# Performance work log

Measured on AMD Instinct MI355X. Metric: run time of the kernel, lower is better.

## Reference

```python
import jax, jax.numpy as jnp
import numpy as np

B, N, D = 64, 1024, 1024

def setup_inputs() -> dict:
    key = jax.random.key(0)
    k1, k2, k3, k4, k5 = jax.random.split(key, 5)
    s = 1.0 / np.sqrt(D)
    return {
        "h_t": jax.random.normal(k1, (B, D), dtype=jnp.float32),
        "keys": jax.random.normal(k2, (B, N, D), dtype=jnp.float32),
        "W_h": jax.random.uniform(k3, (D, D), jnp.float32, -s, s),
        "W_k": jax.random.uniform(k4, (D, D), jnp.float32, -s, s),
        "v": jax.random.uniform(k5, (D,), jnp.float32, -s, s),
    }

def reference(h_t, keys, W_h, W_k, v):
    # W_h(h_t): [B, D]; W_k(keys): [B, N, D]  (nn.Linear computes x @ W.T)
    qh = h_t @ W_h.T                       # [B, D]
    kh = jnp.einsum('bnd,ed->bne', keys, W_k)  # [B, N, D]
    energy = jnp.tanh(qh[:, None, :] + kh)     # [B, N, D]
    scores = jnp.einsum('bnd,d->bn', energy, v)  # [B, N]
    alpha = jax.nn.softmax(scores, axis=-1)      # [B, N]
    context = jnp.einsum('bn,bnd->bd', alpha, keys)  # [B, D]
    return (context, alpha)
```

## Files before the change

### kernel.cpp

```cpp
#include <hip/hip_runtime.h>
#include <math.h>

#define BB 64
#define NN 1024
#define DD 1024

typedef __bf16 bf16x8 __attribute__((ext_vector_type(8)));
typedef _Float16 f16x8 __attribute__((ext_vector_type(8)));
typedef _Float16 f16x4 __attribute__((ext_vector_type(4)));
typedef float f32x4 __attribute__((ext_vector_type(4)));
typedef unsigned short u16x8 __attribute__((ext_vector_type(8)));

#define GLOAD_LDS16(g, l)                                                  \
    __builtin_amdgcn_global_load_lds(                                      \
        (const __attribute__((address_space(1))) unsigned int*)(g),        \
        (__attribute__((address_space(3))) unsigned int*)(l), 16, 0, 0)

__device__ __forceinline__ float fast_tanh(float x) {
    return 1.f - 2.f / (__expf(2.f * x) + 1.f);
}


__global__ __launch_bounds__(256) void cvt_keys(const float* __restrict__ keys,
                                                _Float16* __restrict__ keysT) {
    const int b = blockIdx.y;
    const int nt = blockIdx.x;
    const int t = threadIdx.x;
    const float4* src = (const float4*)(keys + ((size_t)b * NN + nt * 128) * DD);
    _Float16* dst = keysT + (((size_t)b * 8 + nt) * 32) * 4096;
    const int kt = t >> 3;
    const int kc = (t & 7) * 4;
    _Float16* dcol = dst + (size_t)kt * 4096 + kc;
#pragma unroll 4
    for (int n = 0; n < 128; ++n) {
        float4 v4 = src[n * 256 + t];
        f16x4 h = {(_Float16)v4.x, (_Float16)v4.y, (_Float16)v4.z, (_Float16)v4.w};
        *(f16x4*)(dcol + n * 32) = h;
    }
}

__global__ __launch_bounds__(256) void cvt_wk(const float* __restrict__ W_k,
                                              _Float16* __restrict__ wkT) {
    const int et = blockIdx.x;
    const int t = threadIdx.x;
    const float4* src = (const float4*)(W_k + (size_t)et * 128 * DD);
    _Float16* dst = wkT + ((size_t)et * 32) * 4096;
    const int kt = t >> 3;
    const int kc = (t & 7) * 4;
    _Float16* dcol = dst + (size_t)kt * 4096 + kc;
#pragma unroll 4
    for (int n = 0; n < 128; ++n) {
        float4 v4 = src[n * 256 + t];
        f16x4 h = {(_Float16)v4.x, (_Float16)v4.y, (_Float16)v4.z, (_Float16)v4.w};
        *(f16x4*)(dcol + n * 32) = h;
    }
}

__global__ __launch_bounds__(256) void qh_fast(const float* __restrict__ h_t,
                                               const float* __restrict__ W_h,
                                               float* __restrict__ qh,
                                               float* __restrict__ scores) {
    __shared__ float hs[4 * 1024];
    const int ec = blockIdx.x;
    const int bg = blockIdx.y;
    const int t = threadIdx.x;
    const int flat = bg * 4 + ec;
#pragma unroll
    for (int j = 0; j < 4; ++j) scores[flat * 1024 + j * 256 + t] = 0.f;
    const float4* hsrc = (const float4*)(h_t + (size_t)bg * 4 * DD);
    float4* hdst = (float4*)hs;
    for (int i = t; i < 1024; i += 256) hdst[i] = hsrc[i];
    __syncthreads();
    const int e = ec * 256 + t;
    const float4* wrow = (const float4*)(W_h + (size_t)e * DD);
    float a0 = 0.f, a1 = 0.f, a2 = 0.f, a3 = 0.f;
#pragma unroll 2
    for (int k4 = 0; k4 < 256; ++k4) {
        float4 wv = wrow[k4];
        const float* h0 = &hs[4 * k4];
        a0 = fmaf(wv.x, h0[0], a0); a0 = fmaf(wv.y, h0[1], a0);
        a0 = fmaf(wv.z, h0[2], a0); a0 = fmaf(wv.w, h0[3], a0);
        const float* h1 = &hs[1024 + 4 * k4];
        a1 = fmaf(wv.x, h1[0], a1); a1 = fmaf(wv.y, h1[1], a1);
        a1 = fmaf(wv.z, h1[2], a1); a1 = fmaf(wv.w, h1[3], a1);
        const float* h2 = &hs[2048 + 4 * k4];
        a2 = fmaf(wv.x, h2[0], a2); a2 = fmaf(wv.y, h2[1], a2);
        a2 = fmaf(wv.z, h2[2], a2); a2 = fmaf(wv.w, h2[3], a2);
        const float* h3 = &hs[3072 + 4 * k4];
        a3 = fmaf(wv.x, h3[0], a3); a3 = fmaf(wv.y, h3[1], a3);
        a3 = fmaf(wv.z, h3[2], a3); a3 = fmaf(wv.w, h3[3], a3);
    }
    const int b0 = bg * 4;
    qh[(b0 + 0) * DD + e] = a0;
    qh[(b0 + 1) * DD + e] = a1;
    qh[(b0 + 2) * DD + e] = a2;
    qh[(b0 + 3) * DD + e] = a3;
}

__global__ __launch_bounds__(256) void scores_mfma(const _Float16* __restrict__ keysT,
                                                   const _Float16* __restrict__ wkT,
                                                   const float* __restrict__ v,
                                                   const float* __restrict__ qh,
                                                   float* __restrict__ scores) {
    __shared__ _Float16 As[128 * 32];
    __shared__ _Float16 Bs[128 * 32];
    __shared__ float vs[128];
    __shared__ float qs[128];
    __shared__ float red[128][2];

    const int tid = threadIdx.x;
    const int cp = blockIdx.x;
    const int rt = blockIdx.y;
    const int b = rt >> 3;
    const int nt = rt & 7;
    const int e0 = cp * 128;

    if (tid < 128) {
        vs[tid] = v[e0 + tid];
        qs[tid] = qh[b * DD + e0 + tid];
    }

    const char* Abase = (const char*)(keysT + (((size_t)b * 8 + nt) * 32) * 4096);
    const char* Bbase = (const char*)(wkT + ((size_t)cp * 32) * 4096);

    const int w = tid >> 6;
    const int lane = tid & 63;
    const int wm = w & 1;
    const int we = w >> 1;
    const int lcol = lane & 15;
    const int quad = lane >> 4;
    const int soff = w * 2048 + lane * 16;

    f32x4 acc[4][4];
#pragma unroll
    for (int mi = 0; mi < 4; ++mi)
#pragma unroll
        for (int ni = 0; ni < 4; ++ni) acc[mi][ni] = (f32x4){0.f, 0.f, 0.f, 0.f};

    for (int kt = 0; kt < 32; ++kt) {
        __syncthreads();
        const char* ag = Abase + (size_t)kt * 8192 + soff;
        const char* bg = Bbase + (size_t)kt * 8192 + soff;
        char* al_ = (char*)As + soff;
        char* bl_ = (char*)Bs + soff;
        GLOAD_LDS16(ag, al_);
        GLOAD_LDS16(ag + 1024, al_ + 1024);
        GLOAD_LDS16(bg, bl_);
        GLOAD_LDS16(bg + 1024, bl_ + 1024);
        __syncthreads();

        f16x8 af[4], bf[4];
#pragma unroll
        for (int mi = 0; mi < 4; ++mi)
            af[mi] = *(const f16x8*)&As[(wm * 64 + mi * 16 + lcol) * 32 + quad * 8];
#pragma unroll
        for (int ni = 0; ni < 4; ++ni)
            bf[ni] = *(const f16x8*)&Bs[(we * 64 + ni * 16 + lcol) * 32 + quad * 8];
#pragma unroll
        for (int mi = 0; mi < 4; ++mi)
#pragma unroll
            for (int ni = 0; ni < 4; ++ni)
                acc[mi][ni] = __builtin_amdgcn_mfma_f32_16x16x32_f16(af[mi], bf[ni], acc[mi][ni], 0, 0, 0);
    }

    float part[4][4];
#pragma unroll
    for (int mi = 0; mi < 4; ++mi)
#pragma unroll
        for (int r = 0; r < 4; ++r) part[mi][r] = 0.f;
#pragma unroll
    for (int mi = 0; mi < 4; ++mi)
#pragma unroll
        for (int ni = 0; ni < 4; ++ni) {
            const int e = we * 64 + ni * 16 + lcol;
            const float vv = vs[e];
            const float qv = qs[e];
#pragma unroll
            for (int r = 0; r < 4; ++r)
                part[mi][r] += vv * fast_tanh(qv + acc[mi][ni][r]);
        }
#pragma unroll
    for (int mi = 0; mi < 4; ++mi)
#pragma unroll
        for (int r = 0; r < 4; ++r) {
            float p = part[mi][r];
            p += __shfl_xor(p, 1);
            p += __shfl_xor(p, 2);
            p += __shfl_xor(p, 4);
            p += __shfl_xor(p, 8);
            if (lcol == 0) red[wm * 64 + mi * 16 + quad * 4 + r][we] = p;
        }
    __syncthreads();
    if (tid < 128) atomicAdd(&scores[b * NN + nt * 128 + tid], red[tid][0] + red[tid][1]);
}

__global__ __launch_bounds__(256) void softmax_kernel(const float* __restrict__ scores,
                                                      float* __restrict__ alpha,
                                                      float* __restrict__ context) {
    const int b = blockIdx.x;
    const int t = threadIdx.x;
#pragma unroll
    for (int j = 0; j < 4; ++j) context[b * DD + t + 256 * j] = 0.f;
    float x[4];
    float m = -1e30f;
#pragma unroll
    for (int j = 0; j < 4; ++j) {
        x[j] = scores[b * NN + t + 256 * j];
        m = fmaxf(m, x[j]);
    }
#pragma unroll
    for (int mask = 32; mask >= 1; mask >>= 1) m = fmaxf(m, __shfl_xor(m, mask));
    __shared__ float wred[4];
    __shared__ float wsum[4];
    const int wv = t >> 6;
    if ((t & 63) == 0) wred[wv] = m;
    __syncthreads();
    m = fmaxf(fmaxf(wred[0], wred[1]), fmaxf(wred[2], wred[3]));
    float s = 0.f;
#pragma unroll
    for (int j = 0; j < 4; ++j) {
        x[j] = expf(x[j] - m);
        s += x[j];
    }
#pragma unroll
    for (int mask = 32; mask >= 1; mask >>= 1) s += __shfl_xor(s, mask);
    if ((t & 63) == 0) wsum[wv] = s;
    __syncthreads();
    s = wsum[0] + wsum[1] + wsum[2] + wsum[3];
    const float inv = 1.f / s;
#pragma unroll
    for (int j = 0; j < 4; ++j) alpha[b * NN + t + 256 * j] = x[j] * inv;
}

__global__ __launch_bounds__(256) void context_f16(const _Float16* __restrict__ keysT,
                                                   const float* __restrict__ alpha,
                                                   float* __restrict__ context) {
    const int b = blockIdx.y;
    const int nc = blockIdx.x;
    const int t = threadIdx.x;
    __shared__ float al[128];
    if (t < 128) al[t] = alpha[b * NN + nc * 128 + t];
    __syncthreads();
    const _Float16* chunk = keysT + (((size_t)b * 8 + nc) * 32) * 4096;
    const int kt = t >> 3;
    const int kc = (t & 7) * 4;
    const _Float16* p = chunk + (size_t)kt * 4096 + kc;
    float4 acc = {0.f, 0.f, 0.f, 0.f};
#pragma unroll 4
    for (int n = 0; n < 128; ++n) {
        const float a = al[n];
        f16x4 kv = *(const f16x4*)(p + n * 32);
        acc.x = fmaf(a, (float)kv[0], acc.x);
        acc.y = fmaf(a, (float)kv[1], acc.y);
        acc.z = fmaf(a, (float)kv[2], acc.z);
        acc.w = fmaf(a, (float)kv[3], acc.w);
    }
    float* cp = context + b * DD + kt * 32 + kc;
    atomicAdd(cp + 0, acc.x);
    atomicAdd(cp + 1, acc.y);
    atomicAdd(cp + 2, acc.z);
    atomicAdd(cp + 3, acc.w);
}

__global__ __launch_bounds__(256) void qh_fb(const float* __restrict__ h_t,
                                             const float* __restrict__ W_h,
                                             float* __restrict__ qh,
                                             float* __restrict__ scores) {
    __shared__ float hs[DD];
    const int b = blockIdx.y;
    const int e = blockIdx.x * 256 + threadIdx.x;
    scores[(blockIdx.y * 4 + blockIdx.x) * 256 + threadIdx.x] = 0.f;
    for (int i = threadIdx.x; i < DD; i += 256) hs[i] = h_t[b * DD + i];
    __syncthreads();
    const float4* wrow = (const float4*)(W_h + (size_t)e * DD);
    float acc = 0.f;
#pragma unroll 4
    for (int k4 = 0; k4 < DD / 4; ++k4) {
        float4 w = wrow[k4];
        acc = fmaf(w.x, hs[4 * k4 + 0], acc);
        acc = fmaf(w.y, hs[4 * k4 + 1], acc);
        acc = fmaf(w.z, hs[4 * k4 + 2], acc);
        acc = fmaf(w.w, hs[4 * k4 + 3], acc);
    }
    qh[b * DD + e] = acc;
}

#define SPAD 40
__device__ __forceinline__ void split16(const float4* __restrict__ src,
                                        unsigned short* hi, unsigned short* lo) {
    float x[16];
    float4 v0 = src[0], v1 = src[1], v2 = src[2], v3 = src[3];
    x[0] = v0.x; x[1] = v0.y; x[2] = v0.z; x[3] = v0.w;
    x[4] = v1.x; x[5] = v1.y; x[6] = v1.z; x[7] = v1.w;
    x[8] = v2.x; x[9] = v2.y; x[10] = v2.z; x[11] = v2.w;
    x[12] = v3.x; x[13] = v3.y; x[14] = v3.z; x[15] = v3.w;
#pragma unroll
    for (int i = 0; i < 16; ++i) {
        unsigned int u = __float_as_uint(x[i]);
        hi[i] = (unsigned short)(u >> 16);
        float hif = __uint_as_float(u & 0xFFFF0000u);
        float lof = x[i] - hif;
        lo[i] = (unsigned short)(__float_as_uint(lof) >> 16);
    }
}

__global__ __launch_bounds__(256, 2) void scores_fb(const float* __restrict__ keys,
                                                    const float* __restrict__ W_k,
                                                    const float* __restrict__ v,
                                                    const float* __restrict__ qh,
                                                    float* __restrict__ scores) {
    __shared__ unsigned short Ah[128 * SPAD];
    __shared__ unsigned short Al[128 * SPAD];
    __shared__ unsigned short Bh[128 * SPAD];
    __shared__ unsigned short Bl[128 * SPAD];
    __shared__ float vs[128];
    __shared__ float qs[128];
    __shared__ float red[128][2];

    const int tid = threadIdx.x;
    const int cp = blockIdx.x;
    const int rt = blockIdx.y;
    const int b = rt >> 3;
    const int n0 = (rt & 7) * 128;
    const int e0 = cp * 128;
    if (tid < 128) {
        vs[tid] = v[e0 + tid];
        qs[tid] = qh[b * DD + e0 + tid];
    }
    const float* Ag = keys + ((size_t)b * NN + n0) * DD;
    const float* Bg = W_k + (size_t)e0 * DD;
    const int w = tid >> 6;
    const int lane = tid & 63;
    const int wm = w & 1;
    const int we = w >> 1;
    const int lcol = lane & 15;
    const int quad = lane >> 4;
    f32x4 acc[4][4];
#pragma unroll
    for (int mi = 0; mi < 4; ++mi)
#pragma unroll
        for (int ni = 0; ni < 4; ++ni) acc[mi][ni] = (f32x4){0.f, 0.f, 0.f, 0.f};
    const int srow = tid >> 1;
    const int sseg = tid & 1;
    float4 pa[4], pb[4];
    {
        const float4* as = (const float4*)(Ag + (size_t)srow * DD + sseg * 16);
        const float4* bs = (const float4*)(Bg + (size_t)srow * DD + sseg * 16);
#pragma unroll
        for (int i = 0; i < 4; ++i) { pa[i] = as[i]; pb[i] = bs[i]; }
    }
    for (int kt = 0; kt < DD / 32; ++kt) {
        __syncthreads();
        {
            unsigned short hi[16], lo[16];
            split16(pa, hi, lo);
            u16x8* dh = (u16x8*)&Ah[srow * SPAD + sseg * 16];
            u16x8* dl = (u16x8*)&Al[srow * SPAD + sseg * 16];
            dh[0] = *(u16x8*)&hi[0]; dh[1] = *(u16x8*)&hi[8];
            dl[0] = *(u16x8*)&lo[0]; dl[1] = *(u16x8*)&lo[8];
            split16(pb, hi, lo);
            u16x8* eh = (u16x8*)&Bh[srow * SPAD + sseg * 16];
            u16x8* el = (u16x8*)&Bl[srow * SPAD + sseg * 16];
            eh[0] = *(u16x8*)&hi[0]; eh[1] = *(u16x8*)&hi[8];
            el[0] = *(u16x8*)&lo[0]; el[1] = *(u16x8*)&lo[8];
        }
        if (kt + 1 < DD / 32) {
            const int k0 = (kt + 1) * 32;
            const float4* as = (const float4*)(Ag + (size_t)srow * DD + k0 + sseg * 16);
            const float4* bs = (const float4*)(Bg + (size_t)srow * DD + k0 + sseg * 16);
#pragma unroll
            for (int i = 0; i < 4; ++i) { pa[i] = as[i]; pb[i] = bs[i]; }
        }
        __syncthreads();
        bf16x8 ah[4], al2[4], bh[4], bl2[4];
#pragma unroll
        for (int mi = 0; mi < 4; ++mi) {
            const int r = wm * 64 + mi * 16 + lcol;
            ah[mi] = *(const bf16x8*)&Ah[r * SPAD + quad * 8];
            al2[mi] = *(const bf16x8*)&Al[r * SPAD + quad * 8];
        }
#pragma unroll
        for (int ni = 0; ni < 4; ++ni) {
            const int r = we * 64 + ni * 16 + lcol;
            bh[ni] = *(const bf16x8*)&Bh[r * SPAD + quad * 8];
            bl2[ni] = *(const bf16x8*)&Bl[r * SPAD + quad * 8];
        }
#pragma unroll
        for (int mi = 0; mi < 4; ++mi)
#pragma unroll
            for (int ni = 0; ni < 4; ++ni) {
                acc[mi][ni] = __builtin_amdgcn_mfma_f32_16x16x32_bf16(ah[mi], bh[ni], acc[mi][ni], 0, 0, 0);
                acc[mi][ni] = __builtin_amdgcn_mfma_f32_16x16x32_bf16(ah[mi], bl2[ni], acc[mi][ni], 0, 0, 0);
                acc[mi][ni] = __builtin_amdgcn_mfma_f32_16x16x32_bf16(al2[mi], bh[ni], acc[mi][ni], 0, 0, 0);
            }
    }
    float part[4][4];
#pragma unroll
    for (int mi = 0; mi < 4; ++mi)
#pragma unroll
        for (int r = 0; r < 4; ++r) part[mi][r] = 0.f;
#pragma unroll
    for (int mi = 0; mi < 4; ++mi)
#pragma unroll
        for (int ni = 0; ni < 4; ++ni) {
            const int e = we * 64 + ni * 16 + lcol;
            const float vv = vs[e];
            const float qv = qs[e];
#pragma unroll
            for (int r = 0; r < 4; ++r)
                part[mi][r] += vv * fast_tanh(qv + acc[mi][ni][r]);
        }
#pragma unroll
    for (int mi = 0; mi < 4; ++mi)
#pragma unroll
        for (int r = 0; r < 4; ++r) {
            float p = part[mi][r];
            p += __shfl_xor(p, 1);
            p += __shfl_xor(p, 2);
            p += __shfl_xor(p, 4);
            p += __shfl_xor(p, 8);
            if (lcol == 0) red[wm * 64 + mi * 16 + quad * 4 + r][we] = p;
        }
    __syncthreads();
    if (tid < 128) atomicAdd(&scores[b * NN + n0 + tid], red[tid][0] + red[tid][1]);
}

__global__ __launch_bounds__(256) void context_fb(const float* __restrict__ keys,
                                                  const float* __restrict__ alpha,
                                                  float* __restrict__ context) {
    const int b = blockIdx.y;
    const int nc = blockIdx.x;
    const int t = threadIdx.x;
    __shared__ float al[128];
    if (t < 128) al[t] = alpha[b * NN + nc * 128 + t];
    __syncthreads();
    const float4* kp = (const float4*)(keys + ((size_t)b * NN + nc * 128) * DD);
    float4 acc = {0.f, 0.f, 0.f, 0.f};
#pragma unroll 4
    for (int n = 0; n < 128; ++n) {
        const float a = al[n];
        float4 kv = kp[(size_t)n * (DD / 4) + t];
        acc.x = fmaf(a, kv.x, acc.x);
        acc.y = fmaf(a, kv.y, acc.y);
        acc.z = fmaf(a, kv.z, acc.z);
        acc.w = fmaf(a, kv.w, acc.w);
    }
    float* cp = context + b * DD + 4 * t;
    atomicAdd(cp + 0, acc.x);
    atomicAdd(cp + 1, acc.y);
    atomicAdd(cp + 2, acc.z);
    atomicAdd(cp + 3, acc.w);
}

extern "C" void kernel_launch(void* const* d_in, const int* in_sizes, int n_in,
                              void* d_out, int out_size, void* d_ws, size_t ws_size,
                              hipStream_t stream) {
    const float* h_t = (const float*)d_in[0];
    const float* keys = (const float*)d_in[1];
    const float* W_h = (const float*)d_in[2];
    const float* W_k = (const float*)d_in[3];
    const float* v = (const float*)d_in[4];

    float* context = (float*)d_out;
    float* alpha = (float*)d_out + BB * DD;
    float* qh = (float*)d_ws;
    float* scores = (float*)d_ws + BB * DD;

    const size_t wkT_off = (size_t)2 * BB * DD * sizeof(float);
    const size_t keysT_off = wkT_off + (size_t)DD * DD * 2;
    const size_t need = keysT_off + (size_t)BB * NN * DD * 2;

    if (ws_size >= need) {
        _Float16* wkT = (_Float16*)((char*)d_ws + wkT_off);
        _Float16* keysT = (_Float16*)((char*)d_ws + keysT_off);
        cvt_keys<<<dim3(8, BB), 256, 0, stream>>>(keys, keysT);
        cvt_wk<<<dim3(8), 256, 0, stream>>>(W_k, wkT);
        qh_fast<<<dim3(4, 16), 256, 0, stream>>>(h_t, W_h, qh, scores);
        scores_mfma<<<dim3(8, 512), 256, 0, stream>>>(keysT, wkT, v, qh, scores);
        softmax_kernel<<<BB, 256, 0, stream>>>(scores, alpha, context);
        context_f16<<<dim3(8, BB), 256, 0, stream>>>(keysT, alpha, context);
    } else {
        qh_fb<<<dim3(4, BB), 256, 0, stream>>>(h_t, W_h, qh, scores);
        scores_fb<<<dim3(8, 512), 256, 0, stream>>>(keys, W_k, v, qh, scores);
        softmax_kernel<<<BB, 256, 0, stream>>>(scores, alpha, context);
        context_fb<<<dim3(8, BB), 256, 0, stream>>>(keys, alpha, context);
    }
}
```

Before: 677.1 us.

## Merge conversion kernels, double K-step in MFMA loop, rework qh and context

```diff
diff --git a/kernel.cpp b/kernel.cpp
--- a/kernel.cpp
+++ b/kernel.cpp
@@ -21,38 +21,29 @@
 }
 
 
-__global__ __launch_bounds__(256) void cvt_keys(const float* __restrict__ keys,
-                                                _Float16* __restrict__ keysT) {
-    const int b = blockIdx.y;
+__global__ __launch_bounds__(256) void cvt_all(const float* __restrict__ keys,
+                                               const float* __restrict__ W_k,
+                                               _Float16* __restrict__ keysT,
+                                               _Float16* __restrict__ wkT) {
     const int nt = blockIdx.x;
+    const int bb = blockIdx.y;
     const int t = threadIdx.x;
-    const float4* src = (const float4*)(keys + ((size_t)b * NN + nt * 128) * DD);
-    _Float16* dst = keysT + (((size_t)b * 8 + nt) * 32) * 4096;
-    const int kt = t >> 3;
-    const int kc = (t & 7) * 4;
-    _Float16* dcol = dst + (size_t)kt * 4096 + kc;
-#pragma unroll 4
-    for (int n = 0; n < 128; ++n) {
-        float4 v4 = src[n * 256 + t];
-        f16x4 h = {(_Float16)v4.x, (_Float16)v4.y, (_Float16)v4.z, (_Float16)v4.w};
-        *(f16x4*)(dcol + n * 32) = h;
-    }
-}
-
-__global__ __launch_bounds__(256) void cvt_wk(const float* __restrict__ W_k,
-                                              _Float16* __restrict__ wkT) {
-    const int et = blockIdx.x;
-    const int t = threadIdx.x;
-    const float4* src = (const float4*)(W_k + (size_t)et * 128 * DD);
-    _Float16* dst = wkT + ((size_t)et * 32) * 4096;
-    const int kt = t >> 3;
-    const int kc = (t & 7) * 4;
-    _Float16* dcol = dst + (size_t)kt * 4096 + kc;
-#pragma unroll 4
-    for (int n = 0; n < 128; ++n) {
-        float4 v4 = src[n * 256 + t];
-        f16x4 h = {(_Float16)v4.x, (_Float16)v4.y, (_Float16)v4.z, (_Float16)v4.w};
-        *(f16x4*)(dcol + n * 32) = h;
+    const float* src = (bb == 64) ? (W_k + (size_t)nt * 128 * DD)
+                                  : (keys + ((size_t)bb * NN + nt * 128) * DD);
+    _Float16* dst = (bb == 64) ? (wkT + (size_t)nt * 32 * 4096)
+                               : (keysT + (((size_t)bb * 8 + nt) * 32) * 4096);
+    for (int kt = 0; kt < 32; ++kt) {
+#pragma unroll
+        for (int r = 0; r < 2; ++r) {
+            const int p = r * 2048 + t * 8;
+            const int n = p >> 5;
+            const int k = p & 31;
+            const float4* s4 = (const float4*)(src + (size_t)n * DD + kt * 32 + k);
+            float4 a = s4[0], b4 = s4[1];
+            f16x8 h = {(_Float16)a.x,  (_Float16)a.y,  (_Float16)a.z,  (_Float16)a.w,
+                       (_Float16)b4.x, (_Float16)b4.y, (_Float16)b4.z, (_Float16)b4.w};
+            *(f16x8*)(dst + (size_t)kt * 4096 + p) = h;
+        }
     }
 }
 
@@ -60,59 +51,64 @@
                                                const float* __restrict__ W_h,
                                                float* __restrict__ qh,
                                                float* __restrict__ scores) {
-    __shared__ float hs[4 * 1024];
-    const int ec = blockIdx.x;
+    __shared__ float hs[8 * 1024];
+    __shared__ float red2[128][8];
+    const int et = blockIdx.x;
     const int bg = blockIdx.y;
     const int t = threadIdx.x;
-    const int flat = bg * 4 + ec;
-#pragma unroll
-    for (int j = 0; j < 4; ++j) scores[flat * 1024 + j * 256 + t] = 0.f;
-    const float4* hsrc = (const float4*)(h_t + (size_t)bg * 4 * DD);
+    const int bid = bg * 8 + et;
+#pragma unroll
+    for (int j = 0; j < 4; ++j) scores[bid * 1024 + j * 256 + t] = 0.f;
+    const int b0 = bg * 8;
+    const float4* hsrc = (const float4*)(h_t + (size_t)b0 * DD);
     float4* hdst = (float4*)hs;
-    for (int i = t; i < 1024; i += 256) hdst[i] = hsrc[i];
-    __syncthreads();
-    const int e = ec * 256 + t;
-    const float4* wrow = (const float4*)(W_h + (size_t)e * DD);
-    float a0 = 0.f, a1 = 0.f, a2 = 0.f, a3 = 0.f;
-#pragma unroll 2
-    for (int k4 = 0; k4 < 256; ++k4) {
+    for (int i = t; i < 2048; i += 256) hdst[i] = hsrc[i];
+    __syncthreads();
+    const int el = t & 127;
+    const int half = t >> 7;
+    const int e = et * 128 + el;
+    const float4* wrow = (const float4*)(W_h + (size_t)e * DD) + half * 128;
+    float p[8];
+#pragma unroll
+    for (int bi = 0; bi < 8; ++bi) p[bi] = 0.f;
+    for (int k4 = 0; k4 < 128; ++k4) {
         float4 wv = wrow[k4];
-        const float* h0 = &hs[4 * k4];
-        a0 = fmaf(wv.x, h0[0], a0); a0 = fmaf(wv.y, h0[1], a0);
-        a0 = fmaf(wv.z, h0[2], a0); a0 = fmaf(wv.w, h0[3], a0);
-        const float* h1 = &hs[1024 + 4 * k4];
-        a1 = fmaf(wv.x, h1[0], a1); a1 = fmaf(wv.y, h1[1], a1);
-        a1 = fmaf(wv.z, h1[2], a1); a1 = fmaf(wv.w, h1[3], a1);
-        const float* h2 = &hs[2048 + 4 * k4];
-        a2 = fmaf(wv.x, h2[0], a2); a2 = fmaf(wv.y, h2[1], a2);
-        a2 = fmaf(wv.z, h2[2], a2); a2 = fmaf(wv.w, h2[3], a2);
-        const float* h3 = &hs[3072 + 4 * k4];
-        a3 = fmaf(wv.x, h3[0], a3); a3 = fmaf(wv.y, h3[1], a3);
-        a3 = fmaf(wv.z, h3[2], a3); a3 = fmaf(wv.w, h3[3], a3);
-    }
-    const int b0 = bg * 4;
-    qh[(b0 + 0) * DD + e] = a0;
-    qh[(b0 + 1) * DD + e] = a1;
-    qh[(b0 + 2) * DD + e] = a2;
-    qh[(b0 + 3) * DD + e] = a3;
-}
-
-__global__ __launch_bounds__(256) void scores_mfma(const _Float16* __restrict__ keysT,
-                                                   const _Float16* __restrict__ wkT,
-                                                   const float* __restrict__ v,
-                                                   const float* __restrict__ qh,
-                                                   float* __restrict__ scores) {
-    __shared__ _Float16 As[128 * 32];
-    __shared__ _Float16 Bs[128 * 32];
+        const int kb = half * 512 + k4 * 4;
+#pragma unroll
+        for (int bi = 0; bi < 8; ++bi) {
+            const float* hp = &hs[bi * 1024 + kb];
+            p[bi] = fmaf(wv.x, hp[0], p[bi]);
+            p[bi] = fmaf(wv.y, hp[1], p[bi]);
+            p[bi] = fmaf(wv.z, hp[2], p[bi]);
+            p[bi] = fmaf(wv.w, hp[3], p[bi]);
+        }
+    }
+    if (half == 1) {
+#pragma unroll
+        for (int bi = 0; bi < 8; ++bi) red2[el][bi] = p[bi];
+    }
+    __syncthreads();
+    if (half == 0) {
+#pragma unroll
+        for (int bi = 0; bi < 8; ++bi) qh[(size_t)(b0 + bi) * DD + e] = p[bi] + red2[el][bi];
+    }
+}
+
+__global__ __launch_bounds__(256, 4) void scores_mfma(const _Float16* __restrict__ keysT,
+                                                      const _Float16* __restrict__ wkT,
+                                                      const float* __restrict__ v,
+                                                      const float* __restrict__ qh,
+                                                      float* __restrict__ scores) {
+    __shared__ _Float16 As[2 * 128 * 32];
+    __shared__ _Float16 Bs[2 * 128 * 32];
     __shared__ float vs[128];
     __shared__ float qs[128];
     __shared__ float red[128][2];
 
     const int tid = threadIdx.x;
-    const int cp = blockIdx.x;
-    const int rt = blockIdx.y;
-    const int b = rt >> 3;
-    const int nt = rt & 7;
+    const int cp = blockIdx.x >> 3;
+    const int nt = blockIdx.x & 7;
+    const int b = blockIdx.y;
     const int e0 = cp * 128;
 
     if (tid < 128) {
@@ -129,7 +125,7 @@
     const int we = w >> 1;
     const int lcol = lane & 15;
     const int quad = lane >> 4;
-    const int soff = w * 2048 + lane * 16;
+    const int soff = tid * 16;
 
     f32x4 acc[4][4];
 #pragma unroll
@@ -137,30 +133,33 @@
 #pragma unroll
         for (int ni = 0; ni < 4; ++ni) acc[mi][ni] = (f32x4){0.f, 0.f, 0.f, 0.f};
 
-    for (int kt = 0; kt < 32; ++kt) {
+    for (int kt2 = 0; kt2 < 16; ++kt2) {
         __syncthreads();
-        const char* ag = Abase + (size_t)kt * 8192 + soff;
-        const char* bg = Bbase + (size_t)kt * 8192 + soff;
+        const char* ag = Abase + (size_t)kt2 * 16384 + soff;
+        const char* bg = Bbase + (size_t)kt2 * 16384 + soff;
         char* al_ = (char*)As + soff;
         char* bl_ = (char*)Bs + soff;
-        GLOAD_LDS16(ag, al_);
-        GLOAD_LDS16(ag + 1024, al_ + 1024);
-        GLOAD_LDS16(bg, bl_);
-        GLOAD_LDS16(bg + 1024, bl_ + 1024);
+#pragma unroll
+        for (int r = 0; r < 4; ++r) GLOAD_LDS16(ag + r * 4096, al_ + r * 4096);
+#pragma unroll
+        for (int r = 0; r < 4; ++r) GLOAD_LDS16(bg + r * 4096, bl_ + r * 4096);
         __syncthreads();
 
-        f16x8 af[4], bf[4];
-#pragma unroll
-        for (int mi = 0; mi < 4; ++mi)
-            af[mi] = *(const f16x8*)&As[(wm * 64 + mi * 16 + lcol) * 32 + quad * 8];
-#pragma unroll
-        for (int ni = 0; ni < 4; ++ni)
-            bf[ni] = *(const f16x8*)&Bs[(we * 64 + ni * 16 + lcol) * 32 + quad * 8];
-#pragma unroll
-        for (int mi = 0; mi < 4; ++mi)
+#pragma unroll
+        for (int c = 0; c < 2; ++c) {
+            f16x8 af[4], bf[4];
+#pragma unroll
+            for (int mi = 0; mi < 4; ++mi)
+                af[mi] = *(const f16x8*)&As[c * 4096 + (wm * 64 + mi * 16 + lcol) * 32 + quad * 8];
 #pragma unroll
             for (int ni = 0; ni < 4; ++ni)
-                acc[mi][ni] = __builtin_amdgcn_mfma_f32_16x16x32_f16(af[mi], bf[ni], acc[mi][ni], 0, 0, 0);
+                bf[ni] = *(const f16x8*)&Bs[c * 4096 + (we * 64 + ni * 16 + lcol) * 32 + quad * 8];
+#pragma unroll
+            for (int mi = 0; mi < 4; ++mi)
+#pragma unroll
+                for (int ni = 0; ni < 4; ++ni)
+                    acc[mi][ni] = __builtin_amdgcn_mfma_f32_16x16x32_f16(af[mi], bf[ni], acc[mi][ni], 0, 0, 0);
+        }
     }
 
     float part[4][4];
@@ -232,30 +231,27 @@
     for (int j = 0; j < 4; ++j) alpha[b * NN + t + 256 * j] = x[j] * inv;
 }
 
-__global__ __launch_bounds__(256) void context_f16(const _Float16* __restrict__ keysT,
+__global__ __launch_bounds__(256) void context_f32(const float* __restrict__ keys,
                                                    const float* __restrict__ alpha,
                                                    float* __restrict__ context) {
     const int b = blockIdx.y;
     const int nc = blockIdx.x;
     const int t = threadIdx.x;
-    __shared__ float al[128];
-    if (t < 128) al[t] = alpha[b * NN + nc * 128 + t];
-    __syncthreads();
-    const _Float16* chunk = keysT + (((size_t)b * 8 + nc) * 32) * 4096;
-    const int kt = t >> 3;
-    const int kc = (t & 7) * 4;
-    const _Float16* p = chunk + (size_t)kt * 4096 + kc;
+    __shared__ float al[64];
+    if (t < 64) al[t] = alpha[b * NN + nc * 64 + t];
+    __syncthreads();
+    const float4* kp = (const float4*)(keys + ((size_t)b * NN + nc * 64) * DD);
     float4 acc = {0.f, 0.f, 0.f, 0.f};
 #pragma unroll 4
-    for (int n = 0; n < 128; ++n) {
+    for (int n = 0; n < 64; ++n) {
         const float a = al[n];
-        f16x4 kv = *(const f16x4*)(p + n * 32);
-        acc.x = fmaf(a, (float)kv[0], acc.x);
-        acc.y = fmaf(a, (float)kv[1], acc.y);
-        acc.z = fmaf(a, (float)kv[2], acc.z);
-        acc.w = fmaf(a, (float)kv[3], acc.w);
-    }
-    float* cp = context + b * DD + kt * 32 + kc;
+        float4 kv = kp[(size_t)n * (DD / 4) + t];
+        acc.x = fmaf(a, kv.x, acc.x);
+        acc.y = fmaf(a, kv.y, acc.y);
+        acc.z = fmaf(a, kv.z, acc.z);
+        acc.w = fmaf(a, kv.w, acc.w);
+    }
+    float* cp = context + b * DD + 4 * t;
     atomicAdd(cp + 0, acc.x);
     atomicAdd(cp + 1, acc.y);
     atomicAdd(cp + 2, acc.z);
@@ -425,33 +421,6 @@
     if (tid < 128) atomicAdd(&scores[b * NN + n0 + tid], red[tid][0] + red[tid][1]);
 }
 
-__global__ __launch_bounds__(256) void context_fb(const float* __restrict__ keys,
-                                                  const float* __restrict__ alpha,
-                                                  float* __restrict__ context) {
-    const int b = blockIdx.y;
-    const int nc = blockIdx.x;
-    const int t = threadIdx.x;
-    __shared__ float al[128];
-    if (t < 128) al[t] = alpha[b * NN + nc * 128 + t];
-    __syncthreads();
-    const float4* kp = (const float4*)(keys + ((size_t)b * NN + nc * 128) * DD);
-    float4 acc = {0.f, 0.f, 0.f, 0.f};
-#pragma unroll 4
-    for (int n = 0; n < 128; ++n) {
-        const float a = al[n];
-        float4 kv = kp[(size_t)n * (DD / 4) + t];
-        acc.x = fmaf(a, kv.x, acc.x);
-        acc.y = fmaf(a, kv.y, acc.y);
-        acc.z = fmaf(a, kv.z, acc.z);
-        acc.w = fmaf(a, kv.w, acc.w);
-    }
-    float* cp = context + b * DD + 4 * t;
-    atomicAdd(cp + 0, acc.x);
-    atomicAdd(cp + 1, acc.y);
-    atomicAdd(cp + 2, acc.z);
-    atomicAdd(cp + 3, acc.w);
-}
-
 extern "C" void kernel_launch(void* const* d_in, const int* in_sizes, int n_in,
                               void* d_out, int out_size, void* d_ws, size_t ws_size,
                               hipStream_t stream) {
@@ -473,16 +442,15 @@
     if (ws_size >= need) {
         _Float16* wkT = (_Float16*)((char*)d_ws + wkT_off);
         _Float16* keysT = (_Float16*)((char*)d_ws + keysT_off);
-        cvt_keys<<<dim3(8, BB), 256, 0, stream>>>(keys, keysT);
-        cvt_wk<<<dim3(8), 256, 0, stream>>>(W_k, wkT);
-        qh_fast<<<dim3(4, 16), 256, 0, stream>>>(h_t, W_h, qh, scores);
-        scores_mfma<<<dim3(8, 512), 256, 0, stream>>>(keysT, wkT, v, qh, scores);
+        cvt_all<<<dim3(8, 65), 256, 0, stream>>>(keys, W_k, keysT, wkT);
+        qh_fast<<<dim3(8, 8), 256, 0, stream>>>(h_t, W_h, qh, scores);
+        scores_mfma<<<dim3(64, 64), 256, 0, stream>>>(keysT, wkT, v, qh, scores);
         softmax_kernel<<<BB, 256, 0, stream>>>(scores, alpha, context);
-        context_f16<<<dim3(8, BB), 256, 0, stream>>>(keysT, alpha, context);
+        context_f32<<<dim3(16, BB), 256, 0, stream>>>(keys, alpha, context);
     } else {
         qh_fb<<<dim3(4, BB), 256, 0, stream>>>(h_t, W_h, qh, scores);
         scores_fb<<<dim3(8, 512), 256, 0, stream>>>(keys, W_k, v, qh, scores);
         softmax_kernel<<<BB, 256, 0, stream>>>(scores, alpha, context);
-        context_fb<<<dim3(8, BB), 256, 0, stream>>>(keys, alpha, context);
-    }
-}
+        context_f32<<<dim3(16, BB), 256, 0, stream>>>(keys, alpha, context);
+    }
+}
```

New measurement: 646.6 us. 1.05x faster.
